# Optimization experiments

Hardware: AMD Instinct MI355X
Metric: run time of the kernel (lower is better)

Reference implementation:

```python
import jax, jax.numpy as jnp
import numpy as np

B, H, N, D, C, G = 4, 4, 4096, 256, 256, 64  # batch, heads, tokens, emb, channels, grid
EPS = 1e-5


def _layernorm(x, g, b):
    mu = jnp.mean(x, axis=-1, keepdims=True)
    var = jnp.var(x, axis=-1, keepdims=True)
    return (x - mu) * jax.lax.rsqrt(var + EPS) * g + b


def setup_inputs() -> dict:
    key = jax.random.key(0)
    ks = jax.random.split(key, 24)
    s = lambda fan_in: 1.0 / np.sqrt(fan_in)
    inp = {
        "img_emb": jax.random.normal(ks[0], (B, C, G, G), jnp.float32),
        "point_emb": jax.random.normal(ks[1], (B, N, D), jnp.float32),
        # stacked per-head projections (torch Linear: y = x @ W.T + b; store W already transposed)
        "Wq": jax.random.uniform(ks[2], (H, D, D), jnp.float32, -s(D), s(D)),
        "bq": jax.random.uniform(ks[3], (H, D), jnp.float32, -s(D), s(D)),
        "Wk": jax.random.uniform(ks[4], (H, C, D), jnp.float32, -s(C), s(C)),
        "bk": jax.random.uniform(ks[5], (H, D), jnp.float32, -s(C), s(C)),
        "Wv": jax.random.uniform(ks[6], (H, C, D), jnp.float32, -s(C), s(C)),
        "bv": jax.random.uniform(ks[7], (H, D), jnp.float32, -s(C), s(C)),
        "Wo": jax.random.uniform(ks[8], (H * D, D), jnp.float32, -s(H * D), s(H * D)),
        "bo": jax.random.uniform(ks[9], (D,), jnp.float32, -s(H * D), s(H * D)),
        "pos": jax.random.normal(ks[10], (N, D), jnp.float32),
        # FF: 256->128->64->1
        "W1": jax.random.uniform(ks[11], (256, 128), jnp.float32, -s(256), s(256)),
        "b1": jax.random.uniform(ks[12], (128,), jnp.float32, -s(256), s(256)),
        "g1": jnp.ones((128,), jnp.float32),
        "be1": jnp.zeros((128,), jnp.float32),
        "W2": jax.random.uniform(ks[13], (128, 64), jnp.float32, -s(128), s(128)),
        "b2": jax.random.uniform(ks[14], (64,), jnp.float32, -s(128), s(128)),
        "g2": jnp.ones((64,), jnp.float32),
        "be2": jnp.zeros((64,), jnp.float32),
        "W3": jax.random.uniform(ks[15], (64, 1), jnp.float32, -s(64), s(64)),
        "b3": jax.random.uniform(ks[16], (1,), jnp.float32, -s(64), s(64)),
    }
    return inp


def reference(img_emb, point_emb, Wq, bq, Wk, bk, Wv, bv, Wo, bo, pos,
              W1, b1, g1, be1, W2, b2, g2, be2, W3, b3):
    b = img_emb.shape[0]
    # [B, C, G, G] -> [B, N, C]
    img = jnp.transpose(img_emb, (0, 2, 3, 1)).reshape(b, -1, img_emb.shape[1])
    img_pos = img + pos[None, :, :]
    # batched per-head QKV (collapses the per-head Python loop)
    q = jnp.einsum('bnd,hde->bhne', point_emb, Wq) + bq[None, :, None, :]
    k = jnp.einsum('bnc,hce->bhne', img, Wk) + bk[None, :, None, :]
    v = jnp.einsum('bnc,hce->bhne', img_pos, Wv) + bv[None, :, None, :]
    scores = jnp.einsum('bhqe,bhke->bhqk', q, k) / jnp.sqrt(jnp.float32(D))
    attn = jax.nn.softmax(scores, axis=-1)
    att = jnp.einsum('bhqk,bhke->bhqe', attn, v)          # [B, H, N, E]
    att = jnp.transpose(att, (0, 2, 1, 3)).reshape(b, N, H * D)  # concat heads
    emb = att @ Wo + bo + point_emb                        # residual, [B, N, D]
    # small FFN head
    h = _layernorm(jax.nn.relu(emb @ W1 + b1), g1, be1)
    h = _layernorm(jax.nn.relu(h @ W2 + b2), g2, be2)
    act = jax.nn.sigmoid(h @ W3 + b3)                      # [B, N, 1]
    return act, emb
```

## Files before the change

kernel.cpp:

```cpp
#include <hip/hip_runtime.h>

typedef __attribute__((ext_vector_type(8))) short bfrag;
typedef __attribute__((ext_vector_type(8))) unsigned short us8;
typedef __attribute__((ext_vector_type(16))) float f16v;

__device__ __forceinline__ unsigned short f2bf(float f) {
  union { float f; unsigned u; } v; v.f = f;
  unsigned u = v.u;
  return (unsigned short)((u + 0x7fffu + ((u >> 16) & 1u)) >> 16);
}
__device__ __forceinline__ unsigned pkbf(float a, float b) {
  return (unsigned)f2bf(a) | ((unsigned)f2bf(b) << 16);
}
__device__ __forceinline__ unsigned pk2f(float a, float b) {
  union { float f; unsigned u; } ua, ub; ua.f = a; ub.f = b;
  return ((ua.u + 0x8000u) >> 16) | ((ub.u + 0x8000u) & 0xffff0000u);
}
__device__ __forceinline__ float wred(float v) {
#pragma unroll
  for (int m = 32; m >= 1; m >>= 1) v += __shfl_xor(v, m, 64);
  return v;
}

__global__ __launch_bounds__(256) void transp_f2b(
    const float* __restrict__ in, short* __restrict__ out, int R, int Cc)
{
  long zofs = (long)blockIdx.z * R * Cc;
  const float* inz = in + zofs;
  unsigned short* oz = (unsigned short*)out + zofs;
  int i0 = blockIdx.x * 64, j0 = blockIdx.y * 64;
  int l = threadIdx.x & 63, ty = threadIdx.x >> 6;
  int i = i0 + l;
#pragma unroll
  for (int itr = 0; itr < 2; ++itr) {
    int j = j0 + ty * 16 + itr * 8;
    const float* p = inz + (long)i * Cc + j;
    float4 v0 = *(const float4*)(p);
    float4 v1 = *(const float4*)(p + 4);
    float vv[8] = {v0.x, v0.y, v0.z, v0.w, v1.x, v1.y, v1.z, v1.w};
#pragma unroll
    for (int s = 0; s < 8; ++s) oz[(long)(j + s) * R + i] = f2bf(vv[s]);
  }
}

__global__ __launch_bounds__(256) void transp_w3(
    const float* __restrict__ Wq, const float* __restrict__ Wk,
    const float* __restrict__ Wv, short* __restrict__ out)
{
  int z = blockIdx.z;
  const float* inz = (z < 4 ? Wq : (z < 8 ? Wk : Wv)) + (long)(z & 3) * 65536;
  unsigned short* oz = (unsigned short*)out + (long)z * 65536;
  int i0 = blockIdx.x * 64, j0 = blockIdx.y * 64;
  int l = threadIdx.x & 63, ty = threadIdx.x >> 6;
  int i = i0 + l;
#pragma unroll
  for (int itr = 0; itr < 2; ++itr) {
    int j = j0 + ty * 16 + itr * 8;
    const float* p = inz + (long)i * 256 + j;
    float4 v0 = *(const float4*)(p);
    float4 v1 = *(const float4*)(p + 4);
    float vv[8] = {v0.x, v0.y, v0.z, v0.w, v1.x, v1.y, v1.z, v1.w};
#pragma unroll
    for (int s = 0; s < 8; ++s) oz[(long)(j + s) * 256 + i] = f2bf(vv[s]);
  }
}

__global__ __launch_bounds__(256) void transp_img(
    const float* __restrict__ in, const float* __restrict__ pos,
    short* __restrict__ outT, short* __restrict__ outPosT)
{
  long zofs = (long)blockIdx.z * (256L * 4096L);
  const float* inz = in + zofs;
  unsigned short* o1 = (unsigned short*)outT + zofs;
  unsigned short* o2 = (unsigned short*)outPosT + zofs;
  int i0 = blockIdx.x * 64, j0 = blockIdx.y * 64;
  int l = threadIdx.x & 63, ty = threadIdx.x >> 6;
  int i = i0 + l;
#pragma unroll
  for (int itr = 0; itr < 2; ++itr) {
    int j = j0 + ty * 16 + itr * 8;
    const float* p = inz + (long)i * 4096 + j;
    float4 v0 = *(const float4*)(p);
    float4 v1 = *(const float4*)(p + 4);
    float vv[8] = {v0.x, v0.y, v0.z, v0.w, v1.x, v1.y, v1.z, v1.w};
#pragma unroll
    for (int s = 0; s < 8; ++s) {
      float x = vv[s];
      long o = (long)(j + s) * 256 + i;
      o1[o] = f2bf(x);
      o2[o] = f2bf(x + pos[o]);
    }
  }
}

__global__ __launch_bounds__(256) void cast_f2b(
    const float* __restrict__ in, short* __restrict__ out)
{
  long i = ((long)blockIdx.x * 256 + threadIdx.x) * 8;
  float4 v0 = *(const float4*)(in + i);
  float4 v1 = *(const float4*)(in + i + 4);
  uint4 st;
  st.x = pkbf(v0.x, v0.y);
  st.y = pkbf(v0.z, v0.w);
  st.z = pkbf(v1.x, v1.y);
  st.w = pkbf(v1.z, v1.w);
  *(uint4*)((unsigned short*)out + i) = st;
}

__global__ __launch_bounds__(256) void gemm_qkv(
    const short* __restrict__ A, const short* __restrict__ Bt,
    const float* __restrict__ bias, short* __restrict__ Co,
    float scale, int transC)
{
  int z = blockIdx.z;
  const short* Az = A + (long)(z >> 2) * 1048576;
  const short* Btz = Bt + (long)(z & 3) * 65536;
  const float* biasz = bias + (long)(z & 3) * 256;
  short* Cz = Co + (long)z * 1048576;

  int tid = threadIdx.x;
  int w = tid >> 6, lane = tid & 63;
  int half = lane >> 5, ln = lane & 31;
  int wm = w & 1, wn = w >> 1;
  int row0 = blockIdx.x * 128 + wm * 64;
  int col0 = blockIdx.y * 64 + wn * 32;

  f16v acc0, acc1;
#pragma unroll
  for (int i = 0; i < 16; ++i) { acc0[i] = 0.f; acc1[i] = 0.f; }

  const short* ap0 = Az + (long)(row0 + ln) * 256 + half * 8;
  const short* ap1 = Az + (long)(row0 + 32 + ln) * 256 + half * 8;
  const short* bp  = Btz + (long)(col0 + ln) * 256 + half * 8;

#pragma unroll
  for (int kt = 0; kt < 16; ++kt) {
    bfrag a0 = *(const bfrag*)(ap0 + kt * 16);
    bfrag a1 = *(const bfrag*)(ap1 + kt * 16);
    bfrag bb = *(const bfrag*)(bp + kt * 16);
    acc0 = __builtin_amdgcn_mfma_f32_32x32x16_bf16(a0, bb, acc0, 0, 0, 0);
    acc1 = __builtin_amdgcn_mfma_f32_32x32x16_bf16(a1, bb, acc1, 0, 0, 0);
  }

  int col = col0 + ln;
  float bv = biasz[col];
  if (transC) {
#pragma unroll
    for (int t = 0; t < 2; ++t) {
      int rbase = row0 + t * 32;
#pragma unroll
      for (int g = 0; g < 4; ++g) {
        float v0 = ((t ? acc1[4*g+0] : acc0[4*g+0]) + bv) * scale;
        float v1 = ((t ? acc1[4*g+1] : acc0[4*g+1]) + bv) * scale;
        float v2 = ((t ? acc1[4*g+2] : acc0[4*g+2]) + bv) * scale;
        float v3 = ((t ? acc1[4*g+3] : acc0[4*g+3]) + bv) * scale;
        uint2 st;
        st.x = pkbf(v0, v1);
        st.y = pkbf(v2, v3);
        *(uint2*)&((unsigned short*)Cz)[(long)col * 4096 + rbase + 8 * g + 4 * half] = st;
      }
    }
  } else {
#pragma unroll
    for (int t = 0; t < 2; ++t) {
      int rbase = row0 + t * 32;
#pragma unroll
      for (int r = 0; r < 16; ++r) {
        float av = t ? acc1[r] : acc0[r];
        int rr = rbase + (r & 3) + 8 * (r >> 2) + 4 * half;
        ((unsigned short*)Cz)[(long)rr * 256 + col] = f2bf((av + bv) * scale);
      }
    }
  }
}

__global__ __launch_bounds__(256) void gemm_out(
    const short* __restrict__ A, const short* __restrict__ Bt,
    const float* __restrict__ bias, float* __restrict__ Co,
    const float* __restrict__ resid)
{
  int tid = threadIdx.x;
  int w = tid >> 6, lane = tid & 63;
  int half = lane >> 5, ln = lane & 31;
  int wm = w & 1, wn = w >> 1;
  int row0 = blockIdx.x * 128 + wm * 64;
  int col0 = blockIdx.y * 64 + wn * 32;

  f16v acc0, acc1;
#pragma unroll
  for (int i = 0; i < 16; ++i) { acc0[i] = 0.f; acc1[i] = 0.f; }

  int r0 = row0 + ln, r1 = row0 + 32 + ln;
  long a0base = (long)(r0 >> 12) * 4194304 + (long)(r0 & 4095) * 256 + half * 8;
  long a1base = (long)(r1 >> 12) * 4194304 + (long)(r1 & 4095) * 256 + half * 8;
  const short* bp = Bt + (long)(col0 + ln) * 1024 + half * 8;

  for (int kh = 0; kh < 4; ++kh) {
    const short* a0p = A + a0base + (long)kh * 1048576;
    const short* a1p = A + a1base + (long)kh * 1048576;
    const short* bkp = bp + kh * 256;
#pragma unroll
    for (int kt = 0; kt < 16; ++kt) {
      bfrag a0 = *(const bfrag*)(a0p + kt * 16);
      bfrag a1 = *(const bfrag*)(a1p + kt * 16);
      bfrag bb = *(const bfrag*)(bkp + kt * 16);
      acc0 = __builtin_amdgcn_mfma_f32_32x32x16_bf16(a0, bb, acc0, 0, 0, 0);
      acc1 = __builtin_amdgcn_mfma_f32_32x32x16_bf16(a1, bb, acc1, 0, 0, 0);
    }
  }

  int col = col0 + ln;
  float bv = bias[col];
#pragma unroll
  for (int t = 0; t < 2; ++t) {
    int rbase = row0 + t * 32;
#pragma unroll
    for (int r = 0; r < 16; ++r) {
      float av = t ? acc1[r] : acc0[r];
      int rr = rbase + (r & 3) + 8 * (r >> 2) + 4 * half;
      Co[(long)rr * 256 + col] = av + bv + resid[(long)rr * 256 + col];
    }
  }
}

__global__ __launch_bounds__(512) void attn_kernel(
    const short* __restrict__ Qg, const short* __restrict__ Kg,
    const short* __restrict__ Vtg, short* __restrict__ attc)
{
  __shared__ char smem[65536];
  int bx = blockIdx.x;
  int bh = bx & 15, qg = bx >> 4;
  int tid = threadIdx.x;
  int w = tid >> 6, lane = tid & 63;
  int half = lane >> 5, ln = lane & 31;
  int q0 = qg * 256 + w * 32;

  bfrag qf[16];
  {
    const short* qrow = Qg + ((long)bh * 4096 + q0 + ln) * 256 + half * 8;
#pragma unroll
    for (int kt = 0; kt < 16; ++kt) qf[kt] = *(const bfrag*)(qrow + kt * 16);
  }

  int koff[4], voff[2], kst[2], vst[2];
#pragma unroll
  for (int m = 0; m < 4; ++m) koff[m] = ((ln ^ (2 * m + half)) * 16) + half * 512;
#pragma unroll
  for (int kp = 0; kp < 2; ++kp) {
    int ck = 2 * kp + half;
    voff[kp] = 16384 + ck * 4096 + ((ln ^ (ck << 1)) * 16);
  }
#pragma unroll
  for (int p = 0; p < 2; ++p) {
    int u = p * 512 + tid;
    int key = u >> 5, c = u & 31;
    kst[p] = (c * 32 + (key ^ (c & 7))) * 16;
    int e = u >> 2, ck = u & 3;
    vst[p] = 16384 + (ck * 256 + (e ^ (ck << 1))) * 16;
  }

  const char* kg0 = (const char*)Kg + (long)bh * 2097152 + (long)tid * 16;
  const char* kg1 = kg0 + 8192;
  const char* vg0 = (const char*)Vtg + (long)bh * 2097152 +
                    (long)(tid >> 2) * 8192 + (tid & 3) * 16;
  const char* vg1 = vg0 + 1048576;

  f16v O[8];
#pragma unroll
  for (int t = 0; t < 8; ++t)
#pragma unroll
    for (int r = 0; r < 16; ++r) O[t][r] = 0.f;

  float l_run = 0.f;
  union { bfrag f; unsigned u[4]; } bb[2];
  us8 kr[2], vr[2];

  kr[0] = *(const us8*)kg0; kr[1] = *(const us8*)kg1;
  kg0 += 16384; kg1 += 16384;
  *(us8*)(smem + kst[0]) = kr[0];
  *(us8*)(smem + kst[1]) = kr[1];

  __syncthreads();
  kr[0] = *(const us8*)kg0; kr[1] = *(const us8*)kg1;
  kg0 += 16384; kg1 += 16384;
  vr[0] = *(const us8*)vg0; vr[1] = *(const us8*)vg1;
  vg0 += 64; vg1 += 64;
  {
    f16v S;
#pragma unroll
    for (int r = 0; r < 16; ++r) S[r] = 0.f;
#pragma unroll
    for (int kt = 0; kt < 16; ++kt) {
      bfrag a = *(const bfrag*)(smem + koff[kt & 3] + kt * 1024);
      S = __builtin_amdgcn_mfma_f32_32x32x16_bf16(a, qf[kt], S, 0, 0, 0);
    }
    float ss = 0.f;
#pragma unroll
    for (int r = 0; r < 16; ++r) { float e = exp2f(S[r] - 8.f); S[r] = e; ss += e; }
    l_run += ss;
#pragma unroll
    for (int kp = 0; kp < 2; ++kp) {
      unsigned pk0 = pk2f(S[8 * kp + 0], S[8 * kp + 1]);
      unsigned pk1 = pk2f(S[8 * kp + 2], S[8 * kp + 3]);
      unsigned pk2 = pk2f(S[8 * kp + 4], S[8 * kp + 5]);
      unsigned pk3 = pk2f(S[8 * kp + 6], S[8 * kp + 7]);
      unsigned o0 = (unsigned)__shfl_xor((int)pk0, 32);
      unsigned o1 = (unsigned)__shfl_xor((int)pk1, 32);
      unsigned o2 = (unsigned)__shfl_xor((int)pk2, 32);
      unsigned o3 = (unsigned)__shfl_xor((int)pk3, 32);
      bb[kp].u[0] = half ? o2 : pk0;
      bb[kp].u[1] = half ? o3 : pk1;
      bb[kp].u[2] = half ? pk2 : o0;
      bb[kp].u[3] = half ? pk3 : o1;
    }
  }
  *(us8*)(smem + kst[0] + 32768) = kr[0];
  *(us8*)(smem + kst[1] + 32768) = kr[1];
  *(us8*)(smem + vst[0] + 32768) = vr[0];
  *(us8*)(smem + vst[1] + 32768) = vr[1];

#define ATTN_ITER(BUF, KLOAD)                                                  \
  {                                                                            \
    __syncthreads();                                                           \
    if (KLOAD) {                                                               \
      kr[0] = *(const us8*)kg0; kr[1] = *(const us8*)kg1;                      \
      kg0 += 16384; kg1 += 16384;                                              \
    }                                                                          \
    vr[0] = *(const us8*)vg0; vr[1] = *(const us8*)vg1;                        \
    vg0 += 64; vg1 += 64;                                                      \
    f16v S;                                                                    \
    _Pragma("unroll")                                                          \
    for (int r = 0; r < 16; ++r) S[r] = 0.f;                                   \
    _Pragma("unroll")                                                          \
    for (int kt = 0; kt < 16; ++kt) {                                          \
      bfrag a = *(const bfrag*)(smem + koff[kt & 3] + ((BUF)*32768 + kt*1024));\
      S = __builtin_amdgcn_mfma_f32_32x32x16_bf16(a, qf[kt], S, 0, 0, 0);      \
      bfrag va = *(const bfrag*)(smem + voff[kt >> 3] +                        \
                                 ((BUF)*32768 + (kt & 7) * 512));              \
      O[kt & 7] = __builtin_amdgcn_mfma_f32_32x32x16_bf16(va, bb[kt >> 3].f,   \
                                                          O[kt & 7], 0, 0, 0); \
    }                                                                          \
    float ss = 0.f;                                                            \
    _Pragma("unroll")                                                          \
    for (int r = 0; r < 16; ++r) { float e = exp2f(S[r] - 8.f); S[r] = e; ss += e; } \
    l_run += ss;                                                               \
    _Pragma("unroll")                                                          \
    for (int kp = 0; kp < 2; ++kp) {                                           \
      unsigned pk0 = pk2f(S[8 * kp + 0], S[8 * kp + 1]);                       \
      unsigned pk1 = pk2f(S[8 * kp + 2], S[8 * kp + 3]);                       \
      unsigned pk2 = pk2f(S[8 * kp + 4], S[8 * kp + 5]);                       \
      unsigned pk3 = pk2f(S[8 * kp + 6], S[8 * kp + 7]);                       \
      unsigned o0 = (unsigned)__shfl_xor((int)pk0, 32);                        \
      unsigned o1 = (unsigned)__shfl_xor((int)pk1, 32);                        \
      unsigned o2 = (unsigned)__shfl_xor((int)pk2, 32);                        \
      unsigned o3 = (unsigned)__shfl_xor((int)pk3, 32);                        \
      bb[kp].u[0] = half ? o2 : pk0;                                           \
      bb[kp].u[1] = half ? o3 : pk1;                                           \
      bb[kp].u[2] = half ? pk2 : o0;                                           \
      bb[kp].u[3] = half ? pk3 : o1;                                           \
    }                                                                          \
    if (KLOAD) {                                                               \
      *(us8*)(smem + kst[0] + ((BUF) ^ 1) * 32768) = kr[0];                    \
      *(us8*)(smem + kst[1] + ((BUF) ^ 1) * 32768) = kr[1];                    \
    }                                                                          \
    *(us8*)(smem + vst[0] + ((BUF) ^ 1) * 32768) = vr[0];                      \
    *(us8*)(smem + vst[1] + ((BUF) ^ 1) * 32768) = vr[1];                      \
  }

  for (int tp = 0; tp < 63; ++tp) {
    ATTN_ITER(1, 1)
    ATTN_ITER(0, 1)
  }
  ATTN_ITER(1, 0)
#undef ATTN_ITER

  __syncthreads();
#pragma unroll
  for (int kp = 0; kp < 2; ++kp) {
#pragma unroll
    for (int mt = 0; mt < 8; ++mt) {
      bfrag va = *(const bfrag*)(smem + voff[kp] + mt * 512);
      O[mt] = __builtin_amdgcn_mfma_f32_32x32x16_bf16(va, bb[kp].f, O[mt], 0, 0, 0);
    }
  }

  l_run += __shfl_xor(l_run, 32);
  float rl = 1.0f / l_run;
  short* orow = attc + ((long)bh * 4096 + q0 + ln) * 256;
#pragma unroll
  for (int mt = 0; mt < 8; ++mt) {
#pragma unroll
    for (int g = 0; g < 4; ++g) {
      uint2 st;
      st.x = pkbf(O[mt][4 * g + 0] * rl, O[mt][4 * g + 1] * rl);
      st.y = pkbf(O[mt][4 * g + 2] * rl, O[mt][4 * g + 3] * rl);
      *(uint2*)(orow + mt * 32 + 8 * g + 4 * half) = st;
    }
  }
}

__global__ __launch_bounds__(256) void ffn_kernel(
    const float* __restrict__ emb,
    const float* __restrict__ W1, const float* __restrict__ b1,
    const float* __restrict__ g1, const float* __restrict__ be1,
    const float* __restrict__ W2, const float* __restrict__ b2,
    const float* __restrict__ g2, const float* __restrict__ be2,
    const float* __restrict__ W3, const float* __restrict__ b3,
    float* __restrict__ act)
{
  __shared__ float xs[4][256][4];
  __shared__ float hs[4][128][4];
  int w = threadIdx.x >> 6, l = threadIdx.x & 63;
  int row0 = blockIdx.x * 16 + w * 4;
  const float* x = emb + (long)row0 * 256;

  {
    float xv[4][4];
#pragma unroll
    for (int rr = 0; rr < 4; ++rr) {
      float4 t = *(const float4*)(x + rr * 256 + 4 * l);
      xv[0][rr] = t.x; xv[1][rr] = t.y; xv[2][rr] = t.z; xv[3][rr] = t.w;
    }
#pragma unroll
    for (int i = 0; i < 4; ++i) {
      float4 st = make_float4(xv[i][0], xv[i][1], xv[i][2], xv[i][3]);
      *(float4*)&xs[w][4 * l + i][0] = st;
    }
  }

  float a0[4], a1[4];
  {
    float bb0 = b1[2 * l], bb1 = b1[2 * l + 1];
#pragma unroll
    for (int rr = 0; rr < 4; ++rr) { a0[rr] = bb0; a1[rr] = bb1; }
  }
  for (int k = 0; k < 256; ++k) {
    float w0 = W1[k * 128 + 2 * l], w1 = W1[k * 128 + 2 * l + 1];
    float4 xv = *(const float4*)&xs[w][k][0];
    a0[0] += xv.x * w0; a1[0] += xv.x * w1;
    a0[1] += xv.y * w0; a1[1] += xv.y * w1;
    a0[2] += xv.z * w0; a1[2] += xv.z * w1;
    a0[3] += xv.w * w0; a1[3] += xv.w * w1;
  }
  {
    float gg0 = g1[2 * l], gg1 = g1[2 * l + 1];
    float ee0 = be1[2 * l], ee1 = be1[2 * l + 1];
    float n0v[4], n1v[4];
#pragma unroll
    for (int rr = 0; rr < 4; ++rr) {
      float u0 = fmaxf(a0[rr], 0.f), u1 = fmaxf(a1[rr], 0.f);
      float s1 = wred(u0 + u1);
      float s2 = wred(u0 * u0 + u1 * u1);
      float mu = s1 * (1.f / 128.f);
      float var = fmaxf(s2 * (1.f / 128.f) - mu * mu, 0.f);
      float rs = rsqrtf(var + 1e-5f);
      n0v[rr] = (u0 - mu) * rs * gg0 + ee0;
      n1v[rr] = (u1 - mu) * rs * gg1 + ee1;
    }
    *(float4*)&hs[w][2 * l][0]     = make_float4(n0v[0], n0v[1], n0v[2], n0v[3]);
    *(float4*)&hs[w][2 * l + 1][0] = make_float4(n1v[0], n1v[1], n1v[2], n1v[3]);
  }

  float c0[4];
  {
    float bb2 = b2[l];
#pragma unroll
    for (int rr = 0; rr < 4; ++rr) c0[rr] = bb2;
  }
  for (int k = 0; k < 128; ++k) {
    float w2 = W2[k * 64 + l];
    float4 hv = *(const float4*)&hs[w][k][0];
    c0[0] += hv.x * w2;
    c0[1] += hv.y * w2;
    c0[2] += hv.z * w2;
    c0[3] += hv.w * w2;
  }
  {
    float gg2 = g2[l], ee2 = be2[l], w3 = W3[l], bb3 = b3[0];
#pragma unroll
    for (int rr = 0; rr < 4; ++rr) {
      float u = fmaxf(c0[rr], 0.f);
      float t1 = wred(u);
      float t2 = wred(u * u);
      float mu2 = t1 * (1.f / 64.f);
      float var2 = fmaxf(t2 * (1.f / 64.f) - mu2 * mu2, 0.f);
      float rs2 = rsqrtf(var2 + 1e-5f);
      float n2 = (u - mu2) * rs2 * gg2 + ee2;
      float tt = wred(n2 * w3);
      if (l == 0) {
        float r = tt + bb3;
        act[row0 + rr] = 1.f / (1.f + __expf(-r));
      }
    }
  }
}

extern "C" void kernel_launch(void* const* d_in, const int* in_sizes, int n_in,
                              void* d_out, int out_size, void* d_ws, size_t ws_size,
                              hipStream_t stream)
{
  const float* img_emb   = (const float*)d_in[0];
  const float* point_emb = (const float*)d_in[1];
  const float* Wq = (const float*)d_in[2];
  const float* bq = (const float*)d_in[3];
  const float* Wk = (const float*)d_in[4];
  const float* bk = (const float*)d_in[5];
  const float* Wv = (const float*)d_in[6];
  const float* bv = (const float*)d_in[7];
  const float* Wo = (const float*)d_in[8];
  const float* bo = (const float*)d_in[9];
  const float* pos = (const float*)d_in[10];
  const float* W1 = (const float*)d_in[11];
  const float* b1 = (const float*)d_in[12];
  const float* g1 = (const float*)d_in[13];
  const float* be1 = (const float*)d_in[14];
  const float* W2 = (const float*)d_in[15];
  const float* b2 = (const float*)d_in[16];
  const float* g2 = (const float*)d_in[17];
  const float* be2 = (const float*)d_in[18];
  const float* W3 = (const float*)d_in[19];
  const float* b3 = (const float*)d_in[20];

  char* ws = (char*)d_ws;
  short* Qb      = (short*)(ws + 0);
  short* Kb      = (short*)(ws + 33554432);
  short* VtB     = (short*)(ws + 67108864);
  short* peT     = (short*)(ws + 67108864);
  short* imgT    = (short*)(ws + 75497472);
  short* imgPosT = (short*)(ws + 100663296);
  short* WoT     = (short*)(ws + 109051904);
  short* WqT     = (short*)(ws + 109576192);
  short* WkT     = (short*)(ws + 110100480);
  short* WvT     = (short*)(ws + 110624768);
  (void)WkT; (void)WvT;

  float* act_out = (float*)d_out;
  float* emb_out = (float*)d_out + 16384;

  const float qscale = 0.0901684400555602f;

  transp_w3<<<dim3(4, 4, 12), 256, 0, stream>>>(Wq, Wk, Wv, WqT);
  transp_f2b<<<dim3(16, 4, 1), 256, 0, stream>>>(Wo, WoT, 1024, 256);
  transp_img<<<dim3(4, 64, 4), 256, 0, stream>>>(img_emb, pos, imgT, imgPosT);
  cast_f2b<<<2048, 256, 0, stream>>>(point_emb, peT);

  gemm_qkv<<<dim3(32, 4, 16), 256, 0, stream>>>(peT, WqT, bq, Qb, qscale, 0);
  gemm_qkv<<<dim3(32, 4, 16), 256, 0, stream>>>(imgT, WqT + 262144, bk, Kb, 1.0f, 0);
  gemm_qkv<<<dim3(32, 4, 16), 256, 0, stream>>>(imgPosT, WqT + 524288, bv, VtB, 1.0f, 1);

  attn_kernel<<<256, 512, 0, stream>>>(Qb, Kb, VtB, Qb);

  gemm_out<<<dim3(128, 4, 1), 256, 0, stream>>>(Qb, WoT, bo, emb_out, point_emb);

  ffn_kernel<<<1024, 256, 0, stream>>>(emb_out, W1, b1, g1, be1, W2, b2, g2, be2,
                                       W3, b3, act_out);
}
```

Baseline: 639.1 us.

## Stream K/V tiles into LDS with direct global-to-LDS loads

Replaces the register-staged K and V tile loads (global load to VGPRs, then LDS store after compute) with global_load_lds direct DMA into the double-buffered shared memory. The swizzle moves from the LDS store address to the global gather address, so each lane fetches the element that belongs at its linear LDS slot. This removes the staging registers and the trailing ds_write instructions, and launch bounds now request two blocks per CU. Risks include whether the async LDS writes are ordered correctly by the existing barriers and the register pressure implied by the occupancy hint.

```diff
diff --git a/kernel.cpp b/kernel.cpp
--- a/kernel.cpp
+++ b/kernel.cpp
@@ -20,6 +20,11 @@
 #pragma unroll
   for (int m = 32; m >= 1; m >>= 1) v += __shfl_xor(v, m, 64);
   return v;
+}
+__device__ __forceinline__ void dma16(const void* g, void* l) {
+  __builtin_amdgcn_global_load_lds(
+      (const __attribute__((address_space(1))) void*)g,
+      (__attribute__((address_space(3))) void*)l, 16, 0, 0);
 }
 
 __global__ __launch_bounds__(256) void transp_f2b(
@@ -223,7 +228,7 @@
   }
 }
 
-__global__ __launch_bounds__(512) void attn_kernel(
+__global__ __launch_bounds__(512, 2) void attn_kernel(
     const short* __restrict__ Qg, const short* __restrict__ Kg,
     const short* __restrict__ Vtg, short* __restrict__ attc)
 {
@@ -242,7 +247,7 @@
     for (int kt = 0; kt < 16; ++kt) qf[kt] = *(const bfrag*)(qrow + kt * 16);
   }
 
-  int koff[4], voff[2], kst[2], vst[2];
+  int koff[4], voff[2];
 #pragma unroll
   for (int m = 0; m < 4; ++m) koff[m] = ((ln ^ (2 * m + half)) * 16) + half * 512;
 #pragma unroll
@@ -250,20 +255,23 @@
     int ck = 2 * kp + half;
     voff[kp] = 16384 + ck * 4096 + ((ln ^ (ck << 1)) * 16);
   }
-#pragma unroll
-  for (int p = 0; p < 2; ++p) {
-    int u = p * 512 + tid;
-    int key = u >> 5, c = u & 31;
-    kst[p] = (c * 32 + (key ^ (c & 7))) * 16;
-    int e = u >> 2, ck = u & 3;
-    vst[p] = 16384 + (ck * 256 + (e ^ (ck << 1))) * 16;
-  }
-
-  const char* kg0 = (const char*)Kg + (long)bh * 2097152 + (long)tid * 16;
-  const char* kg1 = kg0 + 8192;
-  const char* vg0 = (const char*)Vtg + (long)bh * 2097152 +
-                    (long)(tid >> 2) * 8192 + (tid & 3) * 16;
-  const char* vg1 = vg0 + 1048576;
+
+  int w2 = w * 2;
+  int kgl0, kgl1, vgl0, vgl1;
+  {
+    int c0 = w2 * 2 + half;
+    kgl0 = (ln ^ (c0 & 7)) * 512 + c0 * 16;
+    int c1 = (w2 + 1) * 2 + half;
+    kgl1 = (ln ^ (c1 & 7)) * 512 + c1 * 16;
+    int ck0 = w2 >> 2;
+    int e0 = ((w2 & 3) * 64 + lane) ^ (ck0 << 1);
+    vgl0 = e0 * 8192 + ck0 * 16;
+    int ck1 = (w2 + 1) >> 2;
+    int e1 = (((w2 + 1) & 3) * 64 + lane) ^ (ck1 << 1);
+    vgl1 = e1 * 8192 + ck1 * 16;
+  }
+  const char* kgp = (const char*)Kg + (long)bh * 2097152;
+  const char* vgp = (const char*)Vtg + (long)bh * 2097152;
 
   f16v O[8];
 #pragma unroll
@@ -273,18 +281,18 @@
 
   float l_run = 0.f;
   union { bfrag f; unsigned u[4]; } bb[2];
-  us8 kr[2], vr[2];
-
-  kr[0] = *(const us8*)kg0; kr[1] = *(const us8*)kg1;
-  kg0 += 16384; kg1 += 16384;
-  *(us8*)(smem + kst[0]) = kr[0];
-  *(us8*)(smem + kst[1]) = kr[1];
+
+  dma16(kgp + kgl0, smem + w2 * 1024);
+  dma16(kgp + kgl1, smem + (w2 + 1) * 1024);
+  kgp += 16384;
 
   __syncthreads();
-  kr[0] = *(const us8*)kg0; kr[1] = *(const us8*)kg1;
-  kg0 += 16384; kg1 += 16384;
-  vr[0] = *(const us8*)vg0; vr[1] = *(const us8*)vg1;
-  vg0 += 64; vg1 += 64;
+  dma16(kgp + kgl0, smem + 32768 + w2 * 1024);
+  dma16(kgp + kgl1, smem + 32768 + (w2 + 1) * 1024);
+  kgp += 16384;
+  dma16(vgp + vgl0, smem + 32768 + 16384 + w2 * 1024);
+  dma16(vgp + vgl1, smem + 32768 + 16384 + (w2 + 1) * 1024);
+  vgp += 64;
   {
     f16v S;
 #pragma unroll
@@ -314,20 +322,18 @@
       bb[kp].u[3] = half ? pk3 : o1;
     }
   }
-  *(us8*)(smem + kst[0] + 32768) = kr[0];
-  *(us8*)(smem + kst[1] + 32768) = kr[1];
-  *(us8*)(smem + vst[0] + 32768) = vr[0];
-  *(us8*)(smem + vst[1] + 32768) = vr[1];
 
 #define ATTN_ITER(BUF, KLOAD)                                                  \
   {                                                                            \
     __syncthreads();                                                           \
     if (KLOAD) {                                                               \
-      kr[0] = *(const us8*)kg0; kr[1] = *(const us8*)kg1;                      \
-      kg0 += 16384; kg1 += 16384;                                              \
+      dma16(kgp + kgl0, smem + ((BUF) ^ 1) * 32768 + w2 * 1024);               \
+      dma16(kgp + kgl1, smem + ((BUF) ^ 1) * 32768 + (w2 + 1) * 1024);         \
+      kgp += 16384;                                                            \
     }                                                                          \
-    vr[0] = *(const us8*)vg0; vr[1] = *(const us8*)vg1;                        \
-    vg0 += 64; vg1 += 64;                                                      \
+    dma16(vgp + vgl0, smem + ((BUF) ^ 1) * 32768 + 16384 + w2 * 1024);         \
+    dma16(vgp + vgl1, smem + ((BUF) ^ 1) * 32768 + 16384 + (w2 + 1) * 1024);   \
+    vgp += 64;                                                                 \
     f16v S;                                                                    \
     _Pragma("unroll")                                                          \
     for (int r = 0; r < 16; ++r) S[r] = 0.f;                                   \
@@ -359,12 +365,6 @@
       bb[kp].u[2] = half ? pk2 : o0;                                           \
       bb[kp].u[3] = half ? pk3 : o1;                                           \
     }                                                                          \
-    if (KLOAD) {                                                               \
-      *(us8*)(smem + kst[0] + ((BUF) ^ 1) * 32768) = kr[0];                    \
-      *(us8*)(smem + kst[1] + ((BUF) ^ 1) * 32768) = kr[1];                    \
-    }                                                                          \
-    *(us8*)(smem + vst[0] + ((BUF) ^ 1) * 32768) = vr[0];                      \
-    *(us8*)(smem + vst[1] + ((BUF) ^ 1) * 32768) = vr[1];                      \
   }
 
   for (int tp = 0; tp < 63; ++tp) {
```

Measured after the change: 634.8 us. No clear change (-0.7%).
